# Kernel tuning notes

Hardware: AMD Instinct MI355X
Metric: run time of the kernel (lower is better)

## Reference

```python
import jax, jax.numpy as jnp
import numpy as np

AUX_LOSS_ALPHA = 0.01
TOP_K = 2
N_EXPERTS = 64


def setup_inputs() -> dict:
    key = jax.random.key(0)
    k1, k2 = jax.random.split(key)
    B, S, H, E = 4, 4096, 2048, N_EXPERTS
    hidden_states = jax.random.normal(k1, (B, S, H), dtype=jnp.float32)
    # kaiming_uniform_(a=sqrt(5)) ~ U(-1/sqrt(H), 1/sqrt(H))
    bound = 1.0 / np.sqrt(H)
    weight = jax.random.uniform(k2, (E, H), dtype=jnp.float32, minval=-bound, maxval=bound)
    return {"hidden_states": hidden_states, "weight": weight}


def reference(hidden_states, weight):
    B, S, H = hidden_states.shape
    E, K = N_EXPERTS, TOP_K
    x = hidden_states.reshape(-1, H)              # [T, H], T = B*S
    logits = jnp.einsum('th,eh->te', x, weight)   # router GEMM [T, E]
    scores = jax.nn.softmax(logits, axis=-1)
    topk_weight, topk_idx = jax.lax.top_k(scores, K)  # [T, K]
    # norm_topk_prob (K > 1)
    topk_weight = topk_weight / (jnp.sum(topk_weight, axis=-1, keepdims=True) + 1e-20)
    # seq_aux auxiliary loss (training path)
    idx2d = topk_idx.reshape(B, S * K)            # [B, S*K]
    ce = jnp.zeros((B, E), dtype=scores.dtype)
    ce = ce.at[jnp.arange(B)[:, None], idx2d].add(1.0)
    ce = ce / (S * K / E)
    scores3 = scores.reshape(B, S, E)
    aux_loss = jnp.mean(jnp.sum(ce * jnp.mean(scores3, axis=1), axis=1)) * AUX_LOSS_ALPHA
    return topk_idx, topk_weight, aux_loss
```

## Files before the change

kernel.cpp:

```cpp
#include <hip/hip_runtime.h>
#include <math.h>


#define TT 16384
#define HH 2048
#define EE 64
#define BB 4
#define M_TOK 16
#define KCH 256
#define TAU 2e-3f
#define NREP 8

typedef float v4f __attribute__((ext_vector_type(4)));
typedef float f4v __attribute__((ext_vector_type(4)));
typedef short s8v __attribute__((ext_vector_type(8)));

__device__ __forceinline__ unsigned short f2bf(float f) {
    unsigned u = __float_as_uint(f);
    return (unsigned short)((u + 0x7fffu + ((u >> 16) & 1u)) >> 16);
}
__device__ __forceinline__ float bf2f(unsigned short h) {
    return __uint_as_float(((unsigned)h) << 16);
}

__global__ void prep_b(const float* __restrict__ w,
                       unsigned short* __restrict__ bhi,
                       unsigned short* __restrict__ blo,
                       float* __restrict__ zreg) {
    if (blockIdx.x == 0) {
        for (int i = threadIdx.x; i < 2 * NREP * BB * EE + 16; i += 256) zreg[i] = 0.f;
    }
    int idx = blockIdx.x * blockDim.x + threadIdx.x;
    int j    = idx & 7;
    int lane = (idx >> 3) & 63;
    int ks   = (idx >> 9) & 63;
    int nt   = idx >> 15;
    int e = nt * 16 + (lane & 15);
    int k = ks * 32 + (lane >> 4) * 8 + j;
    float f = w[e * HH + k];
    unsigned short h = f2bf(f);
    bhi[idx] = h;
    blo[idx] = f2bf(f - bf2f(h));
}

__global__ __launch_bounds__(256) void gemm_gate(
    const float* __restrict__ x,
    const unsigned short* __restrict__ bhi, const unsigned short* __restrict__ blo,
    float* __restrict__ logits,
    float* __restrict__ out_idx, float* __restrict__ out_w,
    float* __restrict__ g_cnt, float* __restrict__ g_ssum,
    int* __restrict__ wl_cnt, int* __restrict__ wl) {

    __shared__ unsigned short ahi[2][8 * 64 * 8];
    __shared__ unsigned short alo[2][8 * 64 * 8];
    __shared__ float lg[M_TOK][68];
    __shared__ float bssum[EE];

    const int tid  = threadIdx.x;
    const int wave = tid >> 6;
    const int lane = tid & 63;
    const int tok0 = blockIdx.x * M_TOK;
    const int m  = tid >> 4;
    const int kb = tid & 15;

    if (tid < EE) bssum[tid] = 0.f;

    v4f rx[2][4];

    auto LD = [&](int c, int s) {
        const float* __restrict__ xp = x + (size_t)(tok0 + m) * HH + c * KCH + kb * 8;
        rx[s][0] = *(const v4f*)xp;
        rx[s][1] = *(const v4f*)(xp + 4);
        rx[s][2] = *(const v4f*)(xp + 128);
        rx[s][3] = *(const v4f*)(xp + 132);
    };
    auto ST = [&](int s, int bi) {
#pragma unroll
        for (int g = 0; g < 2; ++g) {
            v4f a = rx[s][g * 2], b2 = rx[s][g * 2 + 1];
            float xs[8] = {a.x, a.y, a.z, a.w, b2.x, b2.y, b2.z, b2.w};
            s8v hv, lv;
#pragma unroll
            for (int j = 0; j < 8; ++j) {
                unsigned short h = f2bf(xs[j]);
                hv[j] = (short)h;
                lv[j] = (short)f2bf(xs[j] - bf2f(h));
            }
            const int k8i = kb + g * 16;
            const int kstep = k8i >> 2, quad = k8i & 3;
            const int entry = kstep * 64 + quad * 16 + (m ^ (quad << 1));
            *(s8v*)&ahi[bi][entry * 8] = hv;
            *(s8v*)&alo[bi][entry * 8] = lv;
        }
    };

    LD(0, 0);
    LD(1, 1);
    ST(0, 0);
    __syncthreads();

    f4v acc = {0.f, 0.f, 0.f, 0.f};
    const int rdl = lane ^ ((lane >> 4) << 1);

#pragma unroll
    for (int c = 0; c < 8; ++c) {
        const int cur = c & 1;
        if (c < 6) LD(c + 2, cur);
        if (c < 7) ST(cur ^ 1, cur ^ 1);
#pragma unroll
        for (int ks = 0; ks < 8; ++ks) {
            const int entry = ks * 64 + rdl;
            s8v af_h = *(const s8v*)&ahi[cur][entry * 8];
            s8v af_l = *(const s8v*)&alo[cur][entry * 8];
            const size_t boff = ((size_t)(wave * 64 + c * 8 + ks) * 64 + lane) * 8;
            s8v bf_h = *(const s8v*)&bhi[boff];
            s8v bf_l = *(const s8v*)&blo[boff];
            acc = __builtin_amdgcn_mfma_f32_16x16x32_bf16(af_h, bf_h, acc, 0, 0, 0);
            acc = __builtin_amdgcn_mfma_f32_16x16x32_bf16(af_h, bf_l, acc, 0, 0, 0);
            acc = __builtin_amdgcn_mfma_f32_16x16x32_bf16(af_l, bf_h, acc, 0, 0, 0);
        }
        __syncthreads();
    }

#pragma unroll
    for (int r = 0; r < 4; ++r) {
        const int row = (lane >> 4) * 4 + r;
        const int col = wave * 16 + (lane & 15);
        lg[row][col] = acc[r];
        logits[(size_t)(tok0 + row) * EE + col] = acc[r];
    }
    __syncthreads();

    const int b   = tok0 >> 12;
    const int rep = (blockIdx.x & (NREP - 1)) * (BB * EE);
    float ssum_l = 0.f;

#pragma unroll
    for (int r = 0; r < 4; ++r) {
        const int tl = wave * 4 + r;
        const int t  = tok0 + tl;
        float l = lg[tl][lane];

        float mx = l;
#pragma unroll
        for (int off = 32; off; off >>= 1) mx = fmaxf(mx, __shfl_xor(mx, off, 64));
        float p = __expf(l - mx);
        float Z = p;
#pragma unroll
        for (int off = 32; off; off >>= 1) Z += __shfl_xor(Z, off, 64);
        ssum_l += p / Z;

        float v = l;
        int cand[3]; float cl[3];
#pragma unroll
        for (int q = 0; q < 3; ++q) {
            float bv = v; int bi = lane;
#pragma unroll
            for (int off = 32; off; off >>= 1) {
                float ov = __shfl_xor(bv, off, 64);
                int   oi = __shfl_xor(bi, off, 64);
                if (ov > bv || (ov == bv && oi < bi)) { bv = ov; bi = oi; }
            }
            cand[q] = bi; cl[q] = bv;
            if (lane == bi) v = -3.4e38f;
        }

        if (lane == 0) {
            atomicAdd(&g_cnt[rep + b * EE + cand[0]], 1.f);
            atomicAdd(&g_cnt[rep + b * EE + cand[1]], 1.f);
            float w1 = 1.f / (1.f + __expf(cl[1] - cl[0]));
            out_idx[t * 2]     = (float)cand[0];
            out_idx[t * 2 + 1] = (float)cand[1];
            out_w[t * 2]       = w1;
            out_w[t * 2 + 1]   = 1.f - w1;
            if (cl[0] - cl[1] < TAU || cl[1] - cl[2] < TAU) {
                int pos = atomicAdd(wl_cnt, 1);
                wl[pos] = t;
            }
        }
    }

    atomicAdd(&bssum[lane], ssum_l);
    __syncthreads();
    if (tid < EE) atomicAdd(&g_ssum[rep + b * EE + tid], bssum[tid]);
}

__global__ __launch_bounds__(256) void rerank_fin(
    const float* __restrict__ logits, const float* __restrict__ x,
    const float* __restrict__ w,
    const int* __restrict__ wl_cnt, const int* __restrict__ wl,
    float* __restrict__ out_idx, float* __restrict__ out_w,
    const float* __restrict__ g_cnt, const float* __restrict__ g_ssum,
    float* __restrict__ aux_out) {

    if (blockIdx.x == 32) {
        if (threadIdx.x < 64) {
            int lane = threadIdx.x;
            float a = 0.f;
            for (int b = 0; b < BB; ++b) {
                float c = 0.f, ss = 0.f;
#pragma unroll
                for (int rr = 0; rr < NREP; ++rr) {
                    c  += g_cnt[rr * (BB * EE) + b * EE + lane];
                    ss += g_ssum[rr * (BB * EE) + b * EE + lane];
                }
                a += c * ss;
            }
#pragma unroll
            for (int off = 32; off; off >>= 1) a += __shfl_xor(a, off, 64);
            if (lane == 0) aux_out[0] = a * (0.01f / (4.f * 128.f * 4096.f));
        }
        return;
    }

    const int lane = threadIdx.x & 63;
    const int wid  = blockIdx.x * 4 + (threadIdx.x >> 6);
    const int n    = wl_cnt[0];

    for (int i = wid; i < n; i += 32 * 4) {
        const int t = wl[i];
        float l = logits[(size_t)t * EE + lane];

        float v = l;
        int cand[4];
#pragma unroll
        for (int r = 0; r < 4; ++r) {
            float bv = v; int bi = lane;
#pragma unroll
            for (int off = 32; off; off >>= 1) {
                float ov = __shfl_xor(bv, off, 64);
                int   oi = __shfl_xor(bi, off, 64);
                if (ov > bv || (ov == bv && oi < bi)) { bv = ov; bi = oi; }
            }
            cand[r] = bi;
            if (lane == bi) v = -3.4e38f;
        }

        const float* __restrict__ xt  = x + (size_t)t * HH;
        const float* __restrict__ w0p = w + (size_t)cand[0] * HH;
        const float* __restrict__ w1p = w + (size_t)cand[1] * HH;
        const float* __restrict__ w2p = w + (size_t)cand[2] * HH;
        const float* __restrict__ w3p = w + (size_t)cand[3] * HH;
        double d0 = 0.0, d1 = 0.0, d2 = 0.0, d3 = 0.0;
#pragma unroll
        for (int ii = 0; ii < 8; ++ii) {
            const int k = ii * 256 + lane * 4;
            v4f xv = *(const v4f*)(xt + k);
            v4f a0 = *(const v4f*)(w0p + k);
            v4f a1 = *(const v4f*)(w1p + k);
            v4f a2 = *(const v4f*)(w2p + k);
            v4f a3 = *(const v4f*)(w3p + k);
            double dx0 = (double)xv.x, dx1 = (double)xv.y;
            double dx2 = (double)xv.z, dx3 = (double)xv.w;
            d0 = fma(dx0, (double)a0.x, d0); d0 = fma(dx1, (double)a0.y, d0);
            d0 = fma(dx2, (double)a0.z, d0); d0 = fma(dx3, (double)a0.w, d0);
            d1 = fma(dx0, (double)a1.x, d1); d1 = fma(dx1, (double)a1.y, d1);
            d1 = fma(dx2, (double)a1.z, d1); d1 = fma(dx3, (double)a1.w, d1);
            d2 = fma(dx0, (double)a2.x, d2); d2 = fma(dx1, (double)a2.y, d2);
            d2 = fma(dx2, (double)a2.z, d2); d2 = fma(dx3, (double)a2.w, d2);
            d3 = fma(dx0, (double)a3.x, d3); d3 = fma(dx1, (double)a3.y, d3);
            d3 = fma(dx2, (double)a3.z, d3); d3 = fma(dx3, (double)a3.w, d3);
        }
#pragma unroll
        for (int off = 32; off; off >>= 1) {
            d0 += __shfl_xor(d0, off, 64);
            d1 += __shfl_xor(d1, off, 64);
            d2 += __shfl_xor(d2, off, 64);
            d3 += __shfl_xor(d3, off, 64);
        }

        double bd[4] = {d0, d1, d2, d3};
        int e1 = cand[0]; double l1 = bd[0];
#pragma unroll
        for (int r = 1; r < 4; ++r)
            if (bd[r] > l1 || (bd[r] == l1 && cand[r] < e1)) { l1 = bd[r]; e1 = cand[r]; }
        int e2 = -1; double l2 = -1e300;
#pragma unroll
        for (int r = 0; r < 4; ++r) {
            if (cand[r] == e1) continue;
            if (e2 < 0 || bd[r] > l2 || (bd[r] == l2 && cand[r] < e2)) { l2 = bd[r]; e2 = cand[r]; }
        }

        double w1 = 1.0 / (1.0 + exp(l2 - l1));
        if (lane == 0) {
            out_idx[t * 2]     = (float)e1;
            out_idx[t * 2 + 1] = (float)e2;
            out_w[t * 2]       = (float)w1;
            out_w[t * 2 + 1]   = (float)(1.0 - w1);
        }
    }
}

extern "C" void kernel_launch(void* const* d_in, const int* in_sizes, int n_in,
                              void* d_out, int out_size, void* d_ws, size_t ws_size,
                              hipStream_t stream) {
    const float* x = (const float*)d_in[0];
    const float* w = (const float*)d_in[1];
    float* out = (float*)d_out;
    float* out_idx = out;
    float* out_w   = out + 2 * TT;
    float* aux     = out + 4 * TT;

    float* logits = (float*)d_ws;
    unsigned short* bhi = (unsigned short*)(logits + (size_t)TT * EE);
    unsigned short* blo = bhi + (size_t)EE * HH;
    float* g_cnt  = (float*)(blo + (size_t)EE * HH);
    float* g_ssum = g_cnt + NREP * BB * EE;
    int*   wl_cnt = (int*)(g_ssum + NREP * BB * EE);
    int*   wl     = wl_cnt + 16;

    prep_b<<<(EE * HH) / 256, 256, 0, stream>>>(w, bhi, blo, g_cnt);
    gemm_gate<<<TT / M_TOK, 256, 0, stream>>>(x, bhi, blo, logits,
                                              out_idx, out_w, g_cnt, g_ssum, wl_cnt, wl);
    rerank_fin<<<33, 256, 0, stream>>>(logits, x, w, wl_cnt, wl,
                                       out_idx, out_w, g_cnt, g_ssum, aux);
}
```

Measured before the change: 231.1 us.

## Fuse rerank and aux-loss finalize into gate GEMM kernel via last-block reduction

Removes the separate rerank_fin launch and the logits write to global memory. Each GEMM block now reranks its own near-tie tokens in fp64 from shared-memory logits, and writes per-block count and score-sum partials. The last block to finish, found with an atomic counter, reduces all partials to produce the aux loss. This drops one launch, the logits round trip and the contended global atomics, at the cost of a serial tail reduction over 1024 partials and uneven per-block rerank work.

```diff
diff --git a/kernel.cpp b/kernel.cpp
--- a/kernel.cpp
+++ b/kernel.cpp
@@ -9,7 +9,7 @@
 #define M_TOK 16
 #define KCH 256
 #define TAU 2e-3f
-#define NREP 8
+#define NBLK (TT / M_TOK)
 
 typedef float v4f __attribute__((ext_vector_type(4)));
 typedef float f4v __attribute__((ext_vector_type(4)));
@@ -26,10 +26,9 @@
 __global__ void prep_b(const float* __restrict__ w,
                        unsigned short* __restrict__ bhi,
                        unsigned short* __restrict__ blo,
-                       float* __restrict__ zreg) {
-    if (blockIdx.x == 0) {
-        for (int i = threadIdx.x; i < 2 * NREP * BB * EE + 16; i += 256) zreg[i] = 0.f;
-    }
+                       int* __restrict__ done) {
+    if (blockIdx.x == 0 && threadIdx.x == 0)
+        __hip_atomic_store(done, 0, __ATOMIC_RELAXED, __HIP_MEMORY_SCOPE_AGENT);
     int idx = blockIdx.x * blockDim.x + threadIdx.x;
     int j    = idx & 7;
     int lane = (idx >> 3) & 63;
@@ -46,15 +45,20 @@
 __global__ __launch_bounds__(256) void gemm_gate(
     const float* __restrict__ x,
     const unsigned short* __restrict__ bhi, const unsigned short* __restrict__ blo,
-    float* __restrict__ logits,
+    const float* __restrict__ w,
     float* __restrict__ out_idx, float* __restrict__ out_w,
-    float* __restrict__ g_cnt, float* __restrict__ g_ssum,
-    int* __restrict__ wl_cnt, int* __restrict__ wl) {
+    float* __restrict__ part, int* __restrict__ done,
+    float* __restrict__ aux_out) {
 
     __shared__ unsigned short ahi[2][8 * 64 * 8];
     __shared__ unsigned short alo[2][8 * 64 * 8];
     __shared__ float lg[M_TOK][68];
     __shared__ float bssum[EE];
+    __shared__ float bcnt[EE];
+    __shared__ int   fl[M_TOK];
+    __shared__ int   fl_cnt;
+    __shared__ int   lastf;
+    __shared__ float warpsum[4];
 
     const int tid  = threadIdx.x;
     const int wave = tid >> 6;
@@ -63,7 +67,8 @@
     const int m  = tid >> 4;
     const int kb = tid & 15;
 
-    if (tid < EE) bssum[tid] = 0.f;
+    if (tid < EE) { bssum[tid] = 0.f; bcnt[tid] = 0.f; }
+    if (tid == 0) fl_cnt = 0;
 
     v4f rx[2][4];
 
@@ -127,12 +132,9 @@
         const int row = (lane >> 4) * 4 + r;
         const int col = wave * 16 + (lane & 15);
         lg[row][col] = acc[r];
-        logits[(size_t)(tok0 + row) * EE + col] = acc[r];
-    }
-    __syncthreads();
-
-    const int b   = tok0 >> 12;
-    const int rep = (blockIdx.x & (NREP - 1)) * (BB * EE);
+    }
+    __syncthreads();
+
     float ssum_l = 0.f;
 
 #pragma unroll
@@ -166,65 +168,45 @@
         }
 
         if (lane == 0) {
-            atomicAdd(&g_cnt[rep + b * EE + cand[0]], 1.f);
-            atomicAdd(&g_cnt[rep + b * EE + cand[1]], 1.f);
+            atomicAdd(&bcnt[cand[0]], 1.f);
+            atomicAdd(&bcnt[cand[1]], 1.f);
             float w1 = 1.f / (1.f + __expf(cl[1] - cl[0]));
             out_idx[t * 2]     = (float)cand[0];
             out_idx[t * 2 + 1] = (float)cand[1];
             out_w[t * 2]       = w1;
             out_w[t * 2 + 1]   = 1.f - w1;
             if (cl[0] - cl[1] < TAU || cl[1] - cl[2] < TAU) {
-                int pos = atomicAdd(wl_cnt, 1);
-                wl[pos] = t;
+                int pos = atomicAdd(&fl_cnt, 1);
+                fl[pos] = tl;
             }
         }
     }
 
     atomicAdd(&bssum[lane], ssum_l);
     __syncthreads();
-    if (tid < EE) atomicAdd(&g_ssum[rep + b * EE + tid], bssum[tid]);
-}
-
-__global__ __launch_bounds__(256) void rerank_fin(
-    const float* __restrict__ logits, const float* __restrict__ x,
-    const float* __restrict__ w,
-    const int* __restrict__ wl_cnt, const int* __restrict__ wl,
-    float* __restrict__ out_idx, float* __restrict__ out_w,
-    const float* __restrict__ g_cnt, const float* __restrict__ g_ssum,
-    float* __restrict__ aux_out) {
-
-    if (blockIdx.x == 32) {
-        if (threadIdx.x < 64) {
-            int lane = threadIdx.x;
-            float a = 0.f;
-            for (int b = 0; b < BB; ++b) {
-                float c = 0.f, ss = 0.f;
-#pragma unroll
-                for (int rr = 0; rr < NREP; ++rr) {
-                    c  += g_cnt[rr * (BB * EE) + b * EE + lane];
-                    ss += g_ssum[rr * (BB * EE) + b * EE + lane];
-                }
-                a += c * ss;
-            }
-#pragma unroll
-            for (int off = 32; off; off >>= 1) a += __shfl_xor(a, off, 64);
-            if (lane == 0) aux_out[0] = a * (0.01f / (4.f * 128.f * 4096.f));
-        }
-        return;
-    }
-
-    const int lane = threadIdx.x & 63;
-    const int wid  = blockIdx.x * 4 + (threadIdx.x >> 6);
-    const int n    = wl_cnt[0];
-
-    for (int i = wid; i < n; i += 32 * 4) {
-        const int t = wl[i];
-        float l = logits[(size_t)t * EE + lane];
+
+    if (tid < 128) {
+        float vv = (tid < 64) ? bcnt[tid] : bssum[tid - 64];
+        __hip_atomic_store(&part[(size_t)blockIdx.x * 128 + tid], vv,
+                           __ATOMIC_RELAXED, __HIP_MEMORY_SCOPE_AGENT);
+    }
+    __syncthreads();
+    if (tid == 0) {
+        int old = __hip_atomic_fetch_add(done, 1, __ATOMIC_ACQ_REL,
+                                         __HIP_MEMORY_SCOPE_AGENT);
+        lastf = (old == NBLK - 1) ? 1 : 0;
+    }
+
+    const int nfl = fl_cnt;
+    for (int i = wave; i < nfl; i += 4) {
+        const int tl = fl[i];
+        const int t  = tok0 + tl;
+        float l = lg[tl][lane];
 
         float v = l;
-        int cand[4];
-#pragma unroll
-        for (int r = 0; r < 4; ++r) {
+        int cand4[4];
+#pragma unroll
+        for (int q = 0; q < 4; ++q) {
             float bv = v; int bi = lane;
 #pragma unroll
             for (int off = 32; off; off >>= 1) {
@@ -232,15 +214,15 @@
                 int   oi = __shfl_xor(bi, off, 64);
                 if (ov > bv || (ov == bv && oi < bi)) { bv = ov; bi = oi; }
             }
-            cand[r] = bi;
+            cand4[q] = bi;
             if (lane == bi) v = -3.4e38f;
         }
 
         const float* __restrict__ xt  = x + (size_t)t * HH;
-        const float* __restrict__ w0p = w + (size_t)cand[0] * HH;
-        const float* __restrict__ w1p = w + (size_t)cand[1] * HH;
-        const float* __restrict__ w2p = w + (size_t)cand[2] * HH;
-        const float* __restrict__ w3p = w + (size_t)cand[3] * HH;
+        const float* __restrict__ w0p = w + (size_t)cand4[0] * HH;
+        const float* __restrict__ w1p = w + (size_t)cand4[1] * HH;
+        const float* __restrict__ w2p = w + (size_t)cand4[2] * HH;
+        const float* __restrict__ w3p = w + (size_t)cand4[3] * HH;
         double d0 = 0.0, d1 = 0.0, d2 = 0.0, d3 = 0.0;
 #pragma unroll
         for (int ii = 0; ii < 8; ++ii) {
@@ -270,24 +252,46 @@
         }
 
         double bd[4] = {d0, d1, d2, d3};
-        int e1 = cand[0]; double l1 = bd[0];
-#pragma unroll
-        for (int r = 1; r < 4; ++r)
-            if (bd[r] > l1 || (bd[r] == l1 && cand[r] < e1)) { l1 = bd[r]; e1 = cand[r]; }
+        int e1 = cand4[0]; double l1 = bd[0];
+#pragma unroll
+        for (int q = 1; q < 4; ++q)
+            if (bd[q] > l1 || (bd[q] == l1 && cand4[q] < e1)) { l1 = bd[q]; e1 = cand4[q]; }
         int e2 = -1; double l2 = -1e300;
 #pragma unroll
-        for (int r = 0; r < 4; ++r) {
-            if (cand[r] == e1) continue;
-            if (e2 < 0 || bd[r] > l2 || (bd[r] == l2 && cand[r] < e2)) { l2 = bd[r]; e2 = cand[r]; }
-        }
-
-        double w1 = 1.0 / (1.0 + exp(l2 - l1));
+        for (int q = 0; q < 4; ++q) {
+            if (cand4[q] == e1) continue;
+            if (e2 < 0 || bd[q] > l2 || (bd[q] == l2 && cand4[q] < e2)) { l2 = bd[q]; e2 = cand4[q]; }
+        }
+
+        double w1d = 1.0 / (1.0 + exp(l2 - l1));
         if (lane == 0) {
             out_idx[t * 2]     = (float)e1;
             out_idx[t * 2 + 1] = (float)e2;
-            out_w[t * 2]       = (float)w1;
-            out_w[t * 2 + 1]   = (float)(1.0 - w1);
-        }
+            out_w[t * 2]       = (float)w1d;
+            out_w[t * 2 + 1]   = (float)(1.0 - w1d);
+        }
+    }
+
+    __syncthreads();
+    if (!lastf) return;
+
+    {
+        const int b = tid >> 6, e = tid & 63;
+        float cnt = 0.f, ssum = 0.f;
+        for (int blk = b * 256; blk < (b + 1) * 256; ++blk) {
+            cnt  += __hip_atomic_load(&part[(size_t)blk * 128 + e],
+                                      __ATOMIC_RELAXED, __HIP_MEMORY_SCOPE_AGENT);
+            ssum += __hip_atomic_load(&part[(size_t)blk * 128 + 64 + e],
+                                      __ATOMIC_RELAXED, __HIP_MEMORY_SCOPE_AGENT);
+        }
+        float a = cnt * ssum;
+#pragma unroll
+        for (int off = 32; off; off >>= 1) a += __shfl_xor(a, off, 64);
+        if ((tid & 63) == 0) warpsum[tid >> 6] = a;
+        __syncthreads();
+        if (tid == 0)
+            aux_out[0] = (warpsum[0] + warpsum[1] + warpsum[2] + warpsum[3])
+                         * (0.01f / (4.f * 128.f * 4096.f));
     }
 }
 
@@ -301,17 +305,12 @@
     float* out_w   = out + 2 * TT;
     float* aux     = out + 4 * TT;
 
-    float* logits = (float*)d_ws;
-    unsigned short* bhi = (unsigned short*)(logits + (size_t)TT * EE);
+    unsigned short* bhi = (unsigned short*)d_ws;
     unsigned short* blo = bhi + (size_t)EE * HH;
-    float* g_cnt  = (float*)(blo + (size_t)EE * HH);
-    float* g_ssum = g_cnt + NREP * BB * EE;
-    int*   wl_cnt = (int*)(g_ssum + NREP * BB * EE);
-    int*   wl     = wl_cnt + 16;
-
-    prep_b<<<(EE * HH) / 256, 256, 0, stream>>>(w, bhi, blo, g_cnt);
-    gemm_gate<<<TT / M_TOK, 256, 0, stream>>>(x, bhi, blo, logits,
-                                              out_idx, out_w, g_cnt, g_ssum, wl_cnt, wl);
-    rerank_fin<<<33, 256, 0, stream>>>(logits, x, w, wl_cnt, wl,
-                                       out_idx, out_w, g_cnt, g_ssum, aux);
-}
+    float* part = (float*)(blo + (size_t)EE * HH);
+    int*   done = (int*)(part + (size_t)NBLK * 128);
+
+    prep_b<<<(EE * HH) / 256, 256, 0, stream>>>(w, bhi, blo, done);
+    gemm_gate<<<NBLK, 256, 0, stream>>>(x, bhi, blo, w, out_idx, out_w,
+                                        part, done, aux);
+}
```

Result: slower. 254.9 us (+10.3%).
